# Performance work log

Measured on AMD Instinct MI355X. Metric: run time of the kernel, lower is better.

## Reference

```python
import jax, jax.numpy as jnp
import numpy as np

# ---- DNC configuration (mirrors access_config / controller_config / args) ----
T, B, IN, OUT = 64, 32, 64, 64          # time, batch, input_size, output_size
N, Wd, R, NW = 128, 64, 4, 1            # memory_size, word_size, num_reads, num_writes
H = 256                                  # controller hidden_size (2 LSTM layers)
CLIP = 20.0
EPS = 1e-6
NUM_MODES = 2 * NW + 1                   # backward modes, forward modes, content mode
IF_SIZES = [R*Wd, R, NW*Wd, NW, NW*Wd, NW*Wd, R, NW, NW, R*NUM_MODES]
IF_SIZE = int(np.sum(IF_SIZES))


def setup_inputs() -> dict:
    key = jax.random.key(0)
    ks = jax.random.split(key, 12)
    in0 = IN + R * Wd  # controller input = external input + flattened prev reads

    def w(k, shape, fan):
        return jax.random.normal(k, shape, jnp.float32) / np.float32(np.sqrt(fan))

    return {
        "inputs": jax.random.normal(ks[0], (T, B, IN), jnp.float32),
        "Wx0": w(ks[1], (in0, 4 * H), in0),
        "Wh0": w(ks[2], (H, 4 * H), H),
        "b0": jnp.zeros((4 * H,), jnp.float32),
        "Wx1": w(ks[3], (H, 4 * H), H),
        "Wh1": w(ks[4], (H, 4 * H), H),
        "b1": jnp.zeros((4 * H,), jnp.float32),
        "W_if": w(ks[5], (H, IF_SIZE), H),
        "b_if": jnp.zeros((IF_SIZE,), jnp.float32),
        "W_out": w(ks[6], (H + R * Wd, OUT), H + R * Wd),
        "b_out": jnp.zeros((OUT,), jnp.float32),
    }


def _lstm(x, h, c, Wx, Wh, b):
    g = x @ Wx + h @ Wh + b
    i, f, gg, o = jnp.split(g, 4, axis=-1)
    c2 = jax.nn.sigmoid(f) * c + jax.nn.sigmoid(i) * jnp.tanh(gg)
    h2 = jax.nn.sigmoid(o) * jnp.tanh(c2)
    return h2, c2


def _content_weights(memory, keys, strengths):
    # memory [B,N,W], keys [B,h,W], strengths [B,h] -> [B,h,N]
    mnorm = jnp.linalg.norm(memory, axis=-1)          # [B,N]
    knorm = jnp.linalg.norm(keys, axis=-1)            # [B,h]
    dot = jnp.einsum('bhw,bnw->bhn', keys, memory)
    sim = dot / (knorm[..., None] * mnorm[:, None, :] + EPS)
    return jax.nn.softmax(sim * strengths[..., None], axis=-1)


def _allocation(usage):
    # usage [B,N] -> allocation weighting [B,N] (DNC freeness-based)
    usage = EPS + (1.0 - EPS) * usage
    order = jnp.argsort(usage, axis=-1)               # ascending usage (most free first)
    sorted_usage = jnp.take_along_axis(usage, order, axis=-1)
    prod = jnp.cumprod(sorted_usage, axis=-1)
    prod_excl = jnp.concatenate([jnp.ones_like(prod[:, :1]), prod[:, :-1]], axis=-1)
    alloc_sorted = (1.0 - sorted_usage) * prod_excl
    inv = jnp.argsort(order, axis=-1)
    return jnp.take_along_axis(alloc_sorted, inv, axis=-1)


def _dnc_forward(inputs, Wx0, Wh0, b0, Wx1, Wh1, b1, W_if, b_if, W_out, b_out):
    eye = 1.0 - jnp.eye(N, dtype=jnp.float32)
    splits = np.cumsum(IF_SIZES)[:-1]

    def step(state, x_t):
        h0, c0, h1, c1, M, rw, ww, link, prec, usage, reads = state
        ctrl_in = jnp.concatenate([x_t, reads.reshape(B, R * Wd)], axis=-1)
        h0, c0 = _lstm(ctrl_in, h0, c0, Wx0, Wh0, b0)
        h1, c1 = _lstm(h0, h1, c1, Wx1, Wh1, b1)
        ctrl = jnp.clip(h1, -CLIP, CLIP)

        p = jnp.split(ctrl @ W_if + b_if, splits, axis=-1)
        read_keys = p[0].reshape(B, R, Wd)
        read_str = 1.0 + jax.nn.softplus(p[1])              # oneplus
        write_keys = p[2].reshape(B, NW, Wd)
        write_str = 1.0 + jax.nn.softplus(p[3])
        erase = jax.nn.sigmoid(p[4]).reshape(B, NW, Wd)
        write_vec = p[5].reshape(B, NW, Wd)
        free_g = jax.nn.sigmoid(p[6])                       # [B,R]
        alloc_g = jax.nn.sigmoid(p[7])                      # [B,NW]
        write_g = jax.nn.sigmoid(p[8])                      # [B,NW]
        modes = jax.nn.softmax(p[9].reshape(B, R, NUM_MODES), axis=-1)

        # -- usage update (prev write weights, then free gates on prev reads) --
        cw = 1.0 - jnp.prod(1.0 - ww, axis=1)               # [B,N]
        u = usage + (1.0 - usage) * cw
        psi = jnp.prod(1.0 - free_g[..., None] * rw, axis=1)
        usage = u * psi

        # -- write weights: content + allocation, gated --
        wc = _content_weights(M, write_keys, write_str)     # [B,NW,N]
        u_tmp = usage
        ww_heads = []
        for i in range(NW):
            a = _allocation(u_tmp)
            wg = write_g[:, i:i+1]
            ag = alloc_g[:, i:i+1]
            ww_heads.append(wg * (ag * a + (1.0 - ag) * wc[:, i]))
            u_tmp = u_tmp + (1.0 - u_tmp) * wg * a
        ww = jnp.stack(ww_heads, axis=1)                    # [B,NW,N]

        # -- erase + write memory --
        erase_m = jnp.prod(1.0 - ww[..., None] * erase[:, :, None, :], axis=1)  # [B,N,W]
        add_m = jnp.einsum('bwn,bwk->bnk', ww, write_vec)
        M = M * erase_m + add_m

        # -- temporal link matrix + precedence --
        wi = ww[..., :, None]
        wj = ww[..., None, :]
        link = ((1.0 - wi - wj) * link + wi * prec[..., None, :]) * eye
        prec = (1.0 - ww.sum(axis=-1, keepdims=True)) * prec + ww

        # -- read weights: backward / content / forward modes --
        rc = _content_weights(M, read_keys, read_str)       # [B,R,N]
        fwd = jnp.einsum('bwij,brj->brwi', link, rw)
        bwd = jnp.einsum('bwji,brj->brwi', link, rw)
        bmode = modes[..., :NW]
        fmode = modes[..., NW:2*NW]
        cmode = modes[..., 2*NW]
        rw = (jnp.einsum('brw,brwn->brn', bmode, bwd)
              + cmode[..., None] * rc
              + jnp.einsum('brw,brwn->brn', fmode, fwd))
        reads = jnp.einsum('brn,bnk->brk', rw, M)           # [B,R,W]

        out = jnp.clip(jnp.concatenate([ctrl, reads.reshape(B, R * Wd)], axis=-1) @ W_out + b_out,
                       -CLIP, CLIP)
        return (h0, c0, h1, c1, M, rw, ww, link, prec, usage, reads), out

    z = jnp.zeros
    init = (z((B, H)), z((B, H)), z((B, H)), z((B, H)),
            z((B, N, Wd)), z((B, R, N)), z((B, NW, N)),
            z((B, NW, N, N)), z((B, NW, N)), z((B, N)), z((B, R, Wd)))
    _, outs = jax.lax.scan(step, init, inputs)
    return outs                                            # [T,B,OUT]


def reference(inputs, Wx0, Wh0, b0, Wx1, Wh1, b1, W_if, b_if, W_out, b_out):
    return _dnc_forward(inputs, Wx0, Wh0, b0, Wx1, Wh1, b1, W_if, b_if, W_out, b_out)
```

## Files before the change

kernel.cpp:

```cpp
#include <hip/hip_runtime.h>
#include <math.h>


#define TT   64
#define BB   32
#define INW  64
#define OUTW 64
#define NN   128
#define WD   64
#define RR   4
#define HH   256
#define IFSZ 471
#define CLIPV 20.0f
#define EPSV  1e-6f
#define NBLK 96

#define OFF_RK   0
#define OFF_RSTR 256
#define OFF_WK   260
#define OFF_WSTR 324
#define OFF_ER   325
#define OFF_WV   389
#define OFF_FG   453
#define OFF_AG   457
#define OFF_WG   458
#define OFF_MD   459

#define S_WSTR 0
#define S_AG   1
#define S_WG   2
#define S_KNW  3
#define S_WSUM 4
#define S_RSTR 8
#define S_FG   12
#define S_KNR  16
#define S_BM   20
#define S_FM   24
#define S_CM   28

#define A_XS   0
#define A_GL   11840
#define A_C0   12896
#define A_GO   13152
#define A_WS   13216
#define A_WO   34528
#define B_XS   0
#define B_GL   9472
#define B_C1   10528
#define B_W1   10784
#define C_MS   0
#define C_LS   8320
#define C_WW   24832
#define C_PRC  24960
#define C_USG  25088
#define C_RWS  25216
#define C_IFC  25728
#define C_FWD  26208
#define C_BWD  26720
#define C_U2   27232
#define C_WCS  27360
#define C_RCS  27488
#define C_MNO  28000
#define C_RDS  28128
#define C_ERS  28384
#define C_WVS  28448
#define C_SC   28512
#define C_SCAL 28576

#define SMEM_FLOATS 36064
#define SMEM_BYTES  (SMEM_FLOATS*4)

#define W_CTL  0
#define W_RDS  8192
#define W_H0   16384
#define W_H1   32768
#define W_FLA  49152
#define W_FLB  (W_FLA + 1024)
#define W_FLC  (W_FLB + 1024)
#define W_END  (W_FLC + 1024)

__device__ __forceinline__ float sigf(float x){ return 1.0f/(1.0f+expf(-x)); }
__device__ __forceinline__ float sofp(float x){ return fmaxf(x,0.0f)+log1pf(expf(-fabsf(x))); }

__device__ __forceinline__ float gload(const float* p){
  return __hip_atomic_load(p, __ATOMIC_RELAXED, __HIP_MEMORY_SCOPE_AGENT);
}
__device__ __forceinline__ void gstore(float* p, float v){
  __hip_atomic_store(p, v, __ATOMIC_RELAXED, __HIP_MEMORY_SCOPE_AGENT);
}

__device__ __forceinline__ void waitflag(const unsigned* slots, unsigned target){
  if (threadIdx.x < 64){
    for (;;){
      unsigned m = __hip_atomic_load(&slots[(threadIdx.x & 31)*32],
                                     __ATOMIC_RELAXED, __HIP_MEMORY_SCOPE_AGENT);
      #pragma unroll
      for (int s=32;s>0;s>>=1){
        unsigned o = (unsigned)__shfl_xor((int)m, s, 64);
        m = (o < m) ? o : m;
      }
      if (m >= target) break;
      __builtin_amdgcn_s_sleep(2);
    }
  }
  __syncthreads();
}

__device__ __forceinline__ void setflag(unsigned* slots, int g, unsigned val){
  asm volatile("s_waitcnt vmcnt(0)" ::: "memory");
  __syncthreads();
  if (threadIdx.x == 0)
    __hip_atomic_store(&slots[g*32], val, __ATOMIC_RELAXED, __HIP_MEMORY_SCOPE_AGENT);
}

__device__ __forceinline__ float wredSum(float v){
  #pragma unroll
  for (int m=32;m>0;m>>=1) v += __shfl_xor(v,m,64);
  return v;
}
__device__ __forceinline__ float wredMax(float v){
  #pragma unroll
  for (int m=32;m>0;m>>=1) v = fmaxf(v,__shfl_xor(v,m,64));
  return v;
}

__device__ __forceinline__ float bfly64(float (&A)[64], int l, int* jb){
  #pragma unroll
  for (int st=0; st<6; ++st){
    const int m = 1<<st, half = 32>>st;
    const bool hi = (l & m) != 0;
    #pragma unroll
    for (int j=0;j<half;j++){
      float a = A[j], b = A[j+half];
      float keep = hi? b : a;
      float send = hi? a : b;
      A[j] = keep + __shfl_xor(send, m, 64);
    }
  }
  *jb = ((l&1)?32:0)|((l&2)?16:0)|((l&4)?8:0)|((l&8)?4:0)|((l&16)?2:0)|((l&32)?1:0);
  return A[0];
}

#define TILE_FMA(WBASE, WROW, XROW)                                      \
  {                                                                      \
    float xv[8], wv[8];                                                  \
    _Pragma("unroll")                                                    \
    for (int q=0;q<8;q++){                                               \
      wv[q] = sm[(WBASE) + (WROW)*37 + c0 + q];                          \
      xv[q] = Xs[(XROW)*37 + b0 + q];                                    \
    }                                                                    \
    _Pragma("unroll")                                                    \
    for (int bi=0;bi<8;bi++)                                             \
      _Pragma("unroll")                                                  \
      for (int ci=0;ci<8;ci++)                                           \
        acc[bi*8+ci] += xv[bi]*wv[ci];                                   \
  }

extern "C" __global__ __launch_bounds__(1024, 1)
void dnc_coop8(const float* __restrict__ inputs,
               const float* __restrict__ Wx0, const float* __restrict__ Wh0, const float* __restrict__ b0g,
               const float* __restrict__ Wx1, const float* __restrict__ Wh1, const float* __restrict__ b1g,
               const float* __restrict__ Wifg, const float* __restrict__ bifg,
               const float* __restrict__ Woutg, const float* __restrict__ boutg,
               float* __restrict__ outg, float* __restrict__ ws)
{
  const int bid  = blockIdx.x;
  const int role = bid >> 5;
  const int g    = bid & 31;
  const int tid  = threadIdx.x;
  const int lane = tid & 63;
  const int wid  = tid >> 6;

  extern __shared__ float sm[];

  float* gctl  = ws + W_CTL;
  float* greads= ws + W_RDS;
  unsigned* fA = (unsigned*)(ws + W_FLA);
  unsigned* fB = (unsigned*)(ws + W_FLB);
  unsigned* fC = (unsigned*)(ws + W_FLC);

  if (role == 0){
    for (int i = tid; i < 576*32; i += 1024){
      int r = i >> 5, cl = i & 31;
      int cglob = 8*g + (cl&7) + ((cl>>3)<<8);
      float v;
      if (r < 256)      v = Wx0[(64+r)*1024 + cglob];
      else if (r < 320) v = Wx0[(r-256)*1024 + cglob];
      else              v = Wh0[(r-320)*1024 + cglob];
      sm[A_WS + r*37 + cl] = v;
    }
    for (int i = tid; i < 512*2; i += 1024){
      int k = i >> 1, c = i & 1;
      sm[A_WO + k*3 + c] = Woutg[k*64 + 2*g + c];
    }
    if (tid < 256) sm[A_C0 + tid] = 0.0f;
  } else if (role == 1){
    for (int i = tid; i < 512*32; i += 1024){
      int r = i >> 5, cl = i & 31;
      int cglob = 8*g + (cl&7) + ((cl>>3)<<8);
      sm[B_W1 + r*37 + cl] = (r < 256) ? Wx1[r*1024 + cglob]
                                       : Wh1[(r-256)*1024 + cglob];
    }
    if (tid < 256) sm[B_C1 + tid] = 0.0f;
  } else {
    for (int i = tid; i < NN*65;  i += 1024) sm[C_MS + i] = 0.0f;
    for (int i = tid; i < NN*129; i += 1024) sm[C_LS + i] = 0.0f;
    if (tid < 128){ sm[C_WW+tid]=0.f; sm[C_PRC+tid]=0.f; sm[C_USG+tid]=0.f; }
    if (tid < 512) sm[C_RWS+tid]=0.f;
  }
  __syncthreads();

  if (role == 0){
    float* Xs = sm + A_XS;
    for (int t = 0; t <= TT; ++t){
      float* h0old = ws + W_H0 + (t&1)*8192;
      float* h0new = ws + W_H0 + ((t+1)&1)*8192;
      float acc[64]; float accO[16];

      waitflag(fA, (unsigned)t);
      if (t < TT){
        for (int i = tid; i < 256*32; i += 1024){
          int k = i>>5, bb = i&31; Xs[k*37+bb] = gload(&h0old[i]);
        }
        for (int i = tid; i < 64*32; i += 1024){
          int bb = i>>6, k = i&63;
          Xs[(256+k)*37+bb] = inputs[(t*BB + bb)*INW + k];
        }
        __syncthreads();
        #pragma unroll
        for (int j=0;j<64;j++) acc[j]=0.f;
        {
          const int b0 = (wid>>2)*8, c0 = (wid&3)*8;
          #pragma unroll
          for (int i=0;i<4;i++){
            int k = i*64 + lane;
            TILE_FMA(A_WS, 320+k, k)
          }
          TILE_FMA(A_WS, 256+lane, 256+lane)
        }
        __syncthreads();
      }
      if (t > 0){
        waitflag(fB, (unsigned)t);
        for (int i = tid; i < 256*32; i += 1024){
          int k = i>>5, bb = i&31; Xs[k*37+bb] = gload(&gctl[i]);
        }
        __syncthreads();
        #pragma unroll
        for (int j=0;j<16;j++) accO[j]=0.f;
        if (wid < 4){
          const int b0 = wid*8;
          #pragma unroll
          for (int i=0;i<4;i++){
            int k = i*64 + lane;
            float w0 = sm[A_WO + k*3], w1 = sm[A_WO + k*3 + 1];
            float xv[8];
            #pragma unroll
            for (int q=0;q<8;q++) xv[q] = Xs[k*37 + b0 + q];
            #pragma unroll
            for (int bi=0;bi<8;bi++){
              accO[bi*2]   += xv[bi]*w0;
              accO[bi*2+1] += xv[bi]*w1;
            }
          }
        }
        __syncthreads();
      }
      waitflag(fC, (unsigned)t);
      for (int i = tid; i < 256*32; i += 1024){
        int k = i>>5, bb = i&31; Xs[k*37+bb] = gload(&greads[i]);
      }
      __syncthreads();
      if (t > 0){
        if (wid < 4){
          const int b0 = wid*8;
          #pragma unroll
          for (int i=0;i<4;i++){
            int k = i*64 + lane;
            float w0 = sm[A_WO + (256+k)*3], w1 = sm[A_WO + (256+k)*3 + 1];
            float xv[8];
            #pragma unroll
            for (int q=0;q<8;q++) xv[q] = Xs[k*37 + b0 + q];
            #pragma unroll
            for (int bi=0;bi<8;bi++){
              accO[bi*2]   += xv[bi]*w0;
              accO[bi*2+1] += xv[bi]*w1;
            }
          }
          #pragma unroll
          for (int st=0; st<4; ++st){
            const int m = 1<<st, half = 8>>st;
            const bool hi = (lane & m) != 0;
            #pragma unroll
            for (int j=0;j<half;j++){
              float a = accO[j], b = accO[j+half];
              float keep = hi? b : a;
              float send = hi? a : b;
              accO[j] = keep + __shfl_xor(send, m, 64);
            }
          }
          accO[0] += __shfl_xor(accO[0], 16, 64);
          accO[0] += __shfl_xor(accO[0], 32, 64);
          int jb = ((lane&1)?8:0)|((lane&2)?4:0)|((lane&4)?2:0)|((lane&8)?1:0);
          if ((lane & 48) == 0){
            int bi = jb>>1, ci = jb&1;
            sm[A_GO + (wid*8+bi)*2 + ci] = accO[0];
          }
        }
        __syncthreads();
        if (tid < 64){
          int bb = tid>>1, c = tid&1;
          float v = sm[A_GO + tid] + boutg[2*g + c];
          outg[((t-1)*BB + bb)*OUTW + 2*g + c] = fminf(CLIPV, fmaxf(-CLIPV, v));
        }
      }
      if (t == TT) break;
      {
        const int b0 = (wid>>2)*8, c0 = (wid&3)*8;
        #pragma unroll
        for (int i=0;i<4;i++){
          int k = i*64 + lane;
          TILE_FMA(A_WS, k, k)
        }
        int jb; float v = bfly64(acc, lane, &jb);
        sm[A_GL + (b0 + (jb>>3))*33 + c0 + (jb&7)] = v;
      }
      __syncthreads();
      if (tid < 256){
        int bb = tid>>3, j = tid&7;
        float gi = sm[A_GL + bb*33 + j]      + b0g[8*g + j];
        float gf = sm[A_GL + bb*33 + 8 + j]  + b0g[256 + 8*g + j];
        float gg = sm[A_GL + bb*33 + 16 + j] + b0g[512 + 8*g + j];
        float go = sm[A_GL + bb*33 + 24 + j] + b0g[768 + 8*g + j];
        float c = sigf(gf)*sm[A_C0+tid] + sigf(gi)*tanhf(gg);
        sm[A_C0+tid] = c;
        gstore(&h0new[(8*g + j)*32 + bb], sigf(go)*tanhf(c));
      }
      setflag(fA, g, (unsigned)(t+1));
    }
  } else if (role == 1){
    float* Xs = sm + B_XS;
    for (int t = 0; t < TT; ++t){
      float* h0new = ws + W_H0 + ((t+1)&1)*8192;
      float* h1old = ws + W_H1 + (t&1)*8192;
      float* h1new = ws + W_H1 + ((t+1)&1)*8192;
      float acc[64];
      #pragma unroll
      for (int j=0;j<64;j++) acc[j]=0.f;

      waitflag(fB, (unsigned)t);
      for (int i = tid; i < 256*32; i += 1024){
        int k = i>>5, bb = i&31; Xs[k*37+bb] = gload(&h1old[i]);
      }
      __syncthreads();
      {
        const int b0 = (wid>>2)*8, c0 = (wid&3)*8;
        #pragma unroll
        for (int i=0;i<4;i++){
          int k = i*64 + lane;
          TILE_FMA(B_W1, 256+k, k)
        }
      }
      __syncthreads();
      waitflag(fA, (unsigned)(t+1));
      for (int i = tid; i < 256*32; i += 1024){
        int k = i>>5, bb = i&31; Xs[k*37+bb] = gload(&h0new[i]);
      }
      __syncthreads();
      {
        const int b0 = (wid>>2)*8, c0 = (wid&3)*8;
        #pragma unroll
        for (int i=0;i<4;i++){
          int k = i*64 + lane;
          TILE_FMA(B_W1, k, k)
        }
        int jb; float v = bfly64(acc, lane, &jb);
        sm[B_GL + (b0 + (jb>>3))*33 + c0 + (jb&7)] = v;
      }
      __syncthreads();
      if (tid < 256){
        int bb = tid>>3, j = tid&7;
        float gi = sm[B_GL + bb*33 + j]      + b1g[8*g + j];
        float gf = sm[B_GL + bb*33 + 8 + j]  + b1g[256 + 8*g + j];
        float gg = sm[B_GL + bb*33 + 16 + j] + b1g[512 + 8*g + j];
        float go = sm[B_GL + bb*33 + 24 + j] + b1g[768 + 8*g + j];
        float c = sigf(gf)*sm[B_C1+tid] + sigf(gi)*tanhf(gg);
        sm[B_C1+tid] = c;
        float h = sigf(go)*tanhf(c);
        gstore(&h1new[(8*g + j)*32 + bb], h);
        gstore(&gctl[(8*g + j)*32 + bb], fminf(CLIPV, fmaxf(-CLIPV, h)));
      }
      setflag(fB, g, (unsigned)(t+1));
    }
  } else {
    float* Ms  = sm + C_MS;
    float* Ls  = sm + C_LS;
    float* wws = sm + C_WW;
    float* prc = sm + C_PRC;
    float* usg = sm + C_USG;
    float* rws = sm + C_RWS;
    float* ifcl= sm + C_IFC;
    float* fwds= sm + C_FWD;
    float* bwds= sm + C_BWD;
    float* u2  = sm + C_U2;
    float* wcs = sm + C_WCS;
    float* rcs = sm + C_RCS;
    float* mno = sm + C_MNO;
    float* rds = sm + C_RDS;
    float* ers = sm + C_ERS;
    float* wvs = sm + C_WVS;
    float* sc  = sm + C_SC;
    float* scal= sm + C_SCAL;
    float* ctl_l = sm + C_RCS;
    float* part  = sm + C_FWD;

    for (int t = 0; t < TT; ++t){
      if (tid < 128){
        int n=tid; float s=0.f;
        #pragma unroll 8
        for (int d=0;d<WD;d++){ float v=Ms[n*65+d]; s+=v*v; }
        mno[n]=sqrtf(s);
      }
      waitflag(fB, (unsigned)(t+1));
      if (tid < 256) ctl_l[tid] = gload(&gctl[tid*32 + g]);
      __syncthreads();
      {
        const int kq = tid >> 9, c = tid & 511;
        if (c < IFSZ){
          const float* Wp = Wifg + (size_t)(kq*128)*IFSZ + c;
          const float* xp = ctl_l + kq*128;
          float a0=0.f, a1=0.f;
          #pragma unroll 8
          for (int k=0;k<128;k+=2){
            a0 += xp[k]   * Wp[(size_t)k*IFSZ];
            a1 += xp[k+1] * Wp[(size_t)(k+1)*IFSZ];
          }
          part[kq*512 + c] = a0 + a1;
        }
      }
      __syncthreads();
      if (tid < IFSZ) ifcl[tid] = part[tid] + part[512+tid] + bifg[tid];
      __syncthreads();

      if (tid < RR){
        scal[S_RSTR+tid]=1.0f+sofp(ifcl[OFF_RSTR+tid]);
        scal[S_FG+tid]  =sigf(ifcl[OFF_FG+tid]);
        float m0=ifcl[OFF_MD+tid*3], m1=ifcl[OFF_MD+tid*3+1], m2=ifcl[OFF_MD+tid*3+2];
        float mx=fmaxf(m0,fmaxf(m1,m2));
        float e0=expf(m0-mx), e1=expf(m1-mx), e2=expf(m2-mx);
        float s=e0+e1+e2;
        scal[S_BM+tid]=e0/s; scal[S_FM+tid]=e1/s; scal[S_CM+tid]=e2/s;
      }
      if (tid == 4) scal[S_WSTR]=1.0f+sofp(ifcl[OFF_WSTR]);
      if (tid == 5) scal[S_AG]=sigf(ifcl[OFF_AG]);
      if (tid == 6) scal[S_WG]=sigf(ifcl[OFF_WG]);
      if (tid >= 64 && tid < 128){
        int d=tid-64;
        ers[d]=sigf(ifcl[OFF_ER+d]);
        wvs[d]=ifcl[OFF_WV+d];
      }
      if (wid == 8){
        float v=ifcl[OFF_WK+lane]; float s=wredSum(v*v);
        if (lane==0) scal[S_KNW]=sqrtf(s);
      }
      if (wid >= 10 && wid < 14){
        int r=wid-10; float v=ifcl[OFF_RK+r*WD+lane]; float s=wredSum(v*v);
        if (lane==0) scal[S_KNR+r]=sqrtf(s);
      }
      __syncthreads();
      if (tid < NN){
        float dot=0.f;
        #pragma unroll 8
        for (int d=0;d<WD;d++) dot += ifcl[OFF_WK+d]*Ms[tid*65+d];
        float sim = dot/(scal[S_KNW]*mno[tid]+EPSV);
        wcs[tid]=sim*scal[S_WSTR];
      }
      __syncthreads();
      if (tid < NN){ float mx=wredMax(wcs[tid]); if(lane==0) sc[wid]=mx; }
      __syncthreads();
      if (tid < NN){
        float mx=fmaxf(sc[0],sc[1]);
        float e=expf(wcs[tid]-mx);
        wcs[tid]=e;
        float s=wredSum(e); if(lane==0) sc[2+wid]=s;
      }
      __syncthreads();
      if (tid < NN) wcs[tid]=wcs[tid]/(sc[2]+sc[3]);
      __syncthreads();
      if (tid < NN){
        float cw = wws[tid];
        float u  = usg[tid] + (1.0f-usg[tid])*cw;
        float psi=1.0f;
        #pragma unroll
        for (int r=0;r<RR;r++) psi *= 1.0f - scal[S_FG+r]*rws[r*NN+tid];
        float us = u*psi;
        usg[tid]=us;
        u2[tid] = EPSV + (1.0f-EPSV)*us;
      }
      __syncthreads();
      if (tid < NN){
        float ui=u2[tid]; float p=1.0f;
        for (int j=0;j<NN;j++){
          float uj=u2[j];
          bool take = (uj<ui) || (uj==ui && j<tid);
          p *= take ? uj : 1.0f;
        }
        float a = (1.0f-ui)*p;
        float wwn = scal[S_WG]*( scal[S_AG]*a + (1.0f-scal[S_AG])*wcs[tid] );
        wws[tid]=wwn;
        float s=wredSum(wwn); if(lane==0) sc[wid]=s;
      }
      __syncthreads();
      if (tid==0) scal[S_WSUM]=sc[0]+sc[1];
      __syncthreads();
      #pragma unroll
      for (int i=0;i<8;i++){
        int el=tid+i*1024, n=el>>6, d=el&63;
        float w=wws[n];
        Ms[n*65+d] = Ms[n*65+d]*(1.0f - w*ers[d]) + w*wvs[d];
      }
      #pragma unroll
      for (int i=0;i<16;i++){
        int el=tid+i*1024, li=el>>7, lj=el&127;
        float v = (li==lj) ? 0.0f
                : (1.0f - wws[li] - wws[lj])*Ls[li*129+lj] + wws[li]*prc[lj];
        Ls[li*129+lj]=v;
      }
      __syncthreads();
      if (tid < NN) prc[tid] = (1.0f - scal[S_WSUM])*prc[tid] + wws[tid];
      if (tid >= 128 && tid < 256){
        int n=tid-128; float s=0.f;
        #pragma unroll 8
        for (int d=0;d<WD;d++){ float v=Ms[n*65+d]; s+=v*v; }
        mno[n]=sqrtf(s);
      }
      __syncthreads();
      if (tid < RR*NN){
        int r=tid>>7, n=tid&127;
        float dot=0.f;
        #pragma unroll 8
        for (int d=0;d<WD;d++) dot += ifcl[OFF_RK+r*WD+d]*Ms[n*65+d];
        float sim = dot/(scal[S_KNR+r]*mno[n]+EPSV);
        rcs[tid]=sim*scal[S_RSTR+r];
      }
      __syncthreads();
      if (tid < RR*NN){ float mx=wredMax(rcs[tid]); if(lane==0) sc[wid]=mx; }
      __syncthreads();
      if (tid < RR*NN){
        int r=tid>>7;
        float mx=fmaxf(sc[r*2],sc[r*2+1]);
        float e=expf(rcs[tid]-mx);
        rcs[tid]=e;
        float s=wredSum(e); if(lane==0) sc[8+wid]=s;
      }
      __syncthreads();
      if (tid < RR*NN){
        int r=tid>>7;
        rcs[tid]=rcs[tid]/(sc[8+r*2]+sc[9+r*2]);
      }
      __syncthreads();
      if (tid < RR*NN){
        int r=tid>>7, i=tid&127;
        float f=0.f, bw=0.f;
        const float* rwr = rws + r*NN;
        #pragma unroll 4
        for (int j=0;j<NN;j++){
          float rv=rwr[j];
          f  += Ls[i*129+j]*rv;
          bw += Ls[j*129+i]*rv;
        }
        fwds[tid]=f; bwds[tid]=bw;
      }
      __syncthreads();
      if (tid < RR*NN){
        int r=tid>>7;
        rws[tid] = scal[S_BM+r]*bwds[tid] + scal[S_CM+r]*rcs[tid] + scal[S_FM+r]*fwds[tid];
      }
      __syncthreads();
      if (tid < RR*WD){
        int r=tid>>6, d=tid&63;
        float s=0.f;
        #pragma unroll 8
        for (int n=0;n<NN;n++) s += rws[r*NN+n]*Ms[n*65+d];
        rds[tid]=s;
      }
      __syncthreads();
      if (tid < 256) gstore(&greads[tid*32 + g], rds[tid]);
      setflag(fC, g, (unsigned)(t+1));
    }
  }
}

extern "C" void kernel_launch(void* const* d_in, const int* in_sizes, int n_in,
                              void* d_out, int out_size, void* d_ws, size_t ws_size,
                              hipStream_t stream)
{
  const float* inputs=(const float*)d_in[0];
  const float* Wx0   =(const float*)d_in[1];
  const float* Wh0   =(const float*)d_in[2];
  const float* b0    =(const float*)d_in[3];
  const float* Wx1   =(const float*)d_in[4];
  const float* Wh1   =(const float*)d_in[5];
  const float* b1    =(const float*)d_in[6];
  const float* Wif   =(const float*)d_in[7];
  const float* bif   =(const float*)d_in[8];
  const float* Wout  =(const float*)d_in[9];
  const float* bout  =(const float*)d_in[10];
  float* out = (float*)d_out;
  float* ws  = (float*)d_ws;

  hipMemsetAsync(ws, 0, W_END * sizeof(float), stream);

  hipFuncSetAttribute((const void*)dnc_coop8,
                      hipFuncAttributeMaxDynamicSharedMemorySize, SMEM_BYTES);

  void* args[] = { (void*)&inputs, (void*)&Wx0, (void*)&Wh0, (void*)&b0,
                   (void*)&Wx1, (void*)&Wh1, (void*)&b1, (void*)&Wif,
                   (void*)&bif, (void*)&Wout, (void*)&bout, (void*)&out,
                   (void*)&ws };
  hipLaunchCooperativeKernel((void*)dnc_coop8, dim3(NBLK), dim3(1024),
                             args, SMEM_BYTES, stream);
}
```

Measured before the change: 3.352 ms.

## Cut barriers in DNC memory step and reorder layer-0 LSTM before output

The memory role's per-step serial chain is restructured. Write and read content softmaxes now run per wavefront using shuffle reductions, independent scalar, usage and erase work runs concurrently in separate waves, memory and link updates are split across wave halves, and forward/backward link products overlap the read content weights. This removes many __syncthreads from the critical recurrent path. In the controller role, layer-0 LSTM for the next step is computed and flagged before the output projection, so downstream blocks can start earlier.

Result: slower. 3.642 ms (+8.7%).

```diff
diff --git a/kernel.cpp b/kernel.cpp
--- a/kernel.cpp
+++ b/kernel.cpp
@@ -26,14 +26,9 @@
 #define OFF_WG   458
 #define OFF_MD   459
 
-#define S_WSTR 0
 #define S_AG   1
 #define S_WG   2
-#define S_KNW  3
 #define S_WSUM 4
-#define S_RSTR 8
-#define S_FG   12
-#define S_KNR  16
 #define S_BM   20
 #define S_FM   24
 #define S_CM   28
@@ -61,10 +56,8 @@
 #define C_WCS  27360
 #define C_RCS  27488
 #define C_MNO  28000
-#define C_RDS  28128
 #define C_ERS  28384
 #define C_WVS  28448
-#define C_SC   28512
 #define C_SCAL 28576
 
 #define SMEM_FLOATS 36064
@@ -113,14 +106,14 @@
     __hip_atomic_store(&slots[g*32], val, __ATOMIC_RELAXED, __HIP_MEMORY_SCOPE_AGENT);
 }
 
-__device__ __forceinline__ float wredSum(float v){
+__device__ __forceinline__ float wmax64(float v){
+  #pragma unroll
+  for (int m=32;m>0;m>>=1) v = fmaxf(v, __shfl_xor(v,m,64));
+  return v;
+}
+__device__ __forceinline__ float wsum64(float v){
   #pragma unroll
   for (int m=32;m>0;m>>=1) v += __shfl_xor(v,m,64);
-  return v;
-}
-__device__ __forceinline__ float wredMax(float v){
-  #pragma unroll
-  for (int m=32;m>0;m>>=1) v = fmaxf(v,__shfl_xor(v,m,64));
   return v;
 }
 
@@ -157,7 +150,7 @@
   }
 
 extern "C" __global__ __launch_bounds__(1024, 1)
-void dnc_coop8(const float* __restrict__ inputs,
+void dnc_coop9(const float* __restrict__ inputs,
                const float* __restrict__ Wx0, const float* __restrict__ Wh0, const float* __restrict__ b0g,
                const float* __restrict__ Wx1, const float* __restrict__ Wh1, const float* __restrict__ b1g,
                const float* __restrict__ Wifg, const float* __restrict__ bifg,
@@ -271,6 +264,30 @@
         int k = i>>5, bb = i&31; Xs[k*37+bb] = gload(&greads[i]);
       }
       __syncthreads();
+      if (t < TT){
+        {
+          const int b0 = (wid>>2)*8, c0 = (wid&3)*8;
+          #pragma unroll
+          for (int i=0;i<4;i++){
+            int k = i*64 + lane;
+            TILE_FMA(A_WS, k, k)
+          }
+          int jb; float v = bfly64(acc, lane, &jb);
+          sm[A_GL + (b0 + (jb>>3))*33 + c0 + (jb&7)] = v;
+        }
+        __syncthreads();
+        if (tid < 256){
+          int bb = tid>>3, j = tid&7;
+          float gi = sm[A_GL + bb*33 + j]      + b0g[8*g + j];
+          float gf = sm[A_GL + bb*33 + 8 + j]  + b0g[256 + 8*g + j];
+          float gg = sm[A_GL + bb*33 + 16 + j] + b0g[512 + 8*g + j];
+          float go = sm[A_GL + bb*33 + 24 + j] + b0g[768 + 8*g + j];
+          float c = sigf(gf)*sm[A_C0+tid] + sigf(gi)*tanhf(gg);
+          sm[A_C0+tid] = c;
+          gstore(&h0new[(8*g + j)*32 + bb], sigf(go)*tanhf(c));
+        }
+        setflag(fA, g, (unsigned)(t+1));
+      }
       if (t > 0){
         if (wid < 4){
           const int b0 = wid*8;
@@ -314,29 +331,6 @@
           outg[((t-1)*BB + bb)*OUTW + 2*g + c] = fminf(CLIPV, fmaxf(-CLIPV, v));
         }
       }
-      if (t == TT) break;
-      {
-        const int b0 = (wid>>2)*8, c0 = (wid&3)*8;
-        #pragma unroll
-        for (int i=0;i<4;i++){
-          int k = i*64 + lane;
-          TILE_FMA(A_WS, k, k)
-        }
-        int jb; float v = bfly64(acc, lane, &jb);
-        sm[A_GL + (b0 + (jb>>3))*33 + c0 + (jb&7)] = v;
-      }
-      __syncthreads();
-      if (tid < 256){
-        int bb = tid>>3, j = tid&7;
-        float gi = sm[A_GL + bb*33 + j]      + b0g[8*g + j];
-        float gf = sm[A_GL + bb*33 + 8 + j]  + b0g[256 + 8*g + j];
-        float gg = sm[A_GL + bb*33 + 16 + j] + b0g[512 + 8*g + j];
-        float go = sm[A_GL + bb*33 + 24 + j] + b0g[768 + 8*g + j];
-        float c = sigf(gf)*sm[A_C0+tid] + sigf(gi)*tanhf(gg);
-        sm[A_C0+tid] = c;
-        gstore(&h0new[(8*g + j)*32 + bb], sigf(go)*tanhf(c));
-      }
-      setflag(fA, g, (unsigned)(t+1));
     }
   } else if (role == 1){
     float* Xs = sm + B_XS;
@@ -406,20 +400,18 @@
     float* wcs = sm + C_WCS;
     float* rcs = sm + C_RCS;
     float* mno = sm + C_MNO;
-    float* rds = sm + C_RDS;
     float* ers = sm + C_ERS;
     float* wvs = sm + C_WVS;
-    float* sc  = sm + C_SC;
     float* scal= sm + C_SCAL;
     float* ctl_l = sm + C_RCS;
     float* part  = sm + C_FWD;
 
     for (int t = 0; t < TT; ++t){
       if (tid < 128){
-        int n=tid; float s=0.f;
+        float s=0.f;
         #pragma unroll 8
-        for (int d=0;d<WD;d++){ float v=Ms[n*65+d]; s+=v*v; }
-        mno[n]=sqrtf(s);
+        for (int d=0;d<WD;d++){ float v=Ms[tid*65+d]; s+=v*v; }
+        mno[tid]=sqrtf(s);
       }
       waitflag(fB, (unsigned)(t+1));
       if (tid < 256) ctl_l[tid] = gload(&gctl[tid*32 + g]);
@@ -442,150 +434,138 @@
       if (tid < IFSZ) ifcl[tid] = part[tid] + part[512+tid] + bifg[tid];
       __syncthreads();
 
-      if (tid < RR){
-        scal[S_RSTR+tid]=1.0f+sofp(ifcl[OFF_RSTR+tid]);
-        scal[S_FG+tid]  =sigf(ifcl[OFF_FG+tid]);
-        float m0=ifcl[OFF_MD+tid*3], m1=ifcl[OFF_MD+tid*3+1], m2=ifcl[OFF_MD+tid*3+2];
-        float mx=fmaxf(m0,fmaxf(m1,m2));
-        float e0=expf(m0-mx), e1=expf(m1-mx), e2=expf(m2-mx);
-        float s=e0+e1+e2;
-        scal[S_BM+tid]=e0/s; scal[S_FM+tid]=e1/s; scal[S_CM+tid]=e2/s;
-      }
-      if (tid == 4) scal[S_WSTR]=1.0f+sofp(ifcl[OFF_WSTR]);
-      if (tid == 5) scal[S_AG]=sigf(ifcl[OFF_AG]);
-      if (tid == 6) scal[S_WG]=sigf(ifcl[OFF_WG]);
-      if (tid >= 64 && tid < 128){
-        int d=tid-64;
-        ers[d]=sigf(ifcl[OFF_ER+d]);
-        wvs[d]=ifcl[OFF_WV+d];
-      }
-      if (wid == 8){
-        float v=ifcl[OFF_WK+lane]; float s=wredSum(v*v);
-        if (lane==0) scal[S_KNW]=sqrtf(s);
-      }
-      if (wid >= 10 && wid < 14){
-        int r=wid-10; float v=ifcl[OFF_RK+r*WD+lane]; float s=wredSum(v*v);
-        if (lane==0) scal[S_KNR+r]=sqrtf(s);
-      }
-      __syncthreads();
-      if (tid < NN){
-        float dot=0.f;
+      if (wid == 0){
+        int n1 = lane, n2 = lane + 64;
+        float d1=0.f, d2=0.f, kn=0.f;
         #pragma unroll 8
-        for (int d=0;d<WD;d++) dot += ifcl[OFF_WK+d]*Ms[tid*65+d];
-        float sim = dot/(scal[S_KNW]*mno[tid]+EPSV);
-        wcs[tid]=sim*scal[S_WSTR];
-      }
-      __syncthreads();
-      if (tid < NN){ float mx=wredMax(wcs[tid]); if(lane==0) sc[wid]=mx; }
-      __syncthreads();
-      if (tid < NN){
-        float mx=fmaxf(sc[0],sc[1]);
-        float e=expf(wcs[tid]-mx);
-        wcs[tid]=e;
-        float s=wredSum(e); if(lane==0) sc[2+wid]=s;
-      }
-      __syncthreads();
-      if (tid < NN) wcs[tid]=wcs[tid]/(sc[2]+sc[3]);
-      __syncthreads();
-      if (tid < NN){
-        float cw = wws[tid];
-        float u  = usg[tid] + (1.0f-usg[tid])*cw;
-        float psi=1.0f;
+        for (int d=0; d<WD; ++d){
+          float wk = ifcl[OFF_WK+d];
+          d1 += wk*Ms[n1*65+d];
+          d2 += wk*Ms[n2*65+d];
+          kn += wk*wk;
+        }
+        float wstr = 1.0f + sofp(ifcl[OFF_WSTR]);
+        float knr = sqrtf(kn);
+        float s1 = d1/(knr*mno[n1]+EPSV)*wstr;
+        float s2 = d2/(knr*mno[n2]+EPSV)*wstr;
+        float mx = wmax64(fmaxf(s1,s2));
+        float e1 = expf(s1-mx), e2 = expf(s2-mx);
+        float sum = wsum64(e1+e2);
+        wcs[n1] = e1/sum; wcs[n2] = e2/sum;
+      } else if (wid == 1){
+        if (lane < 4){
+          float m0=ifcl[OFF_MD+lane*3], m1=ifcl[OFF_MD+lane*3+1], m2=ifcl[OFF_MD+lane*3+2];
+          float mx=fmaxf(m0,fmaxf(m1,m2));
+          float e0=expf(m0-mx), e1=expf(m1-mx), e2=expf(m2-mx);
+          float s=e0+e1+e2;
+          scal[S_BM+lane]=e0/s; scal[S_FM+lane]=e1/s; scal[S_CM+lane]=e2/s;
+        }
+        if (lane == 4) scal[S_AG]=sigf(ifcl[OFF_AG]);
+        if (lane == 5) scal[S_WG]=sigf(ifcl[OFF_WG]);
+      } else if (wid == 2 || wid == 3){
+        int n = tid - 128;
+        float cw = wws[n];
+        float u  = usg[n] + (1.0f-usg[n])*cw;
+        float psi = 1.0f;
         #pragma unroll
-        for (int r=0;r<RR;r++) psi *= 1.0f - scal[S_FG+r]*rws[r*NN+tid];
+        for (int r=0;r<RR;r++) psi *= 1.0f - sigf(ifcl[OFF_FG+r])*rws[r*NN+n];
         float us = u*psi;
-        usg[tid]=us;
-        u2[tid] = EPSV + (1.0f-EPSV)*us;
-      }
-      __syncthreads();
-      if (tid < NN){
-        float ui=u2[tid]; float p=1.0f;
+        usg[n] = us;
+        u2[n]  = EPSV + (1.0f-EPSV)*us;
+      } else if (wid == 4){
+        ers[lane] = sigf(ifcl[OFF_ER+lane]);
+        wvs[lane] = ifcl[OFF_WV+lane];
+      }
+      __syncthreads();
+
+      if (wid == 0){
+        int n1 = lane, n2 = lane + 64;
+        float uA = u2[n1], uB = u2[n2];
+        float p1 = 1.0f, p2 = 1.0f;
         for (int j=0;j<NN;j++){
-          float uj=u2[j];
-          bool take = (uj<ui) || (uj==ui && j<tid);
-          p *= take ? uj : 1.0f;
-        }
-        float a = (1.0f-ui)*p;
-        float wwn = scal[S_WG]*( scal[S_AG]*a + (1.0f-scal[S_AG])*wcs[tid] );
-        wws[tid]=wwn;
-        float s=wredSum(wwn); if(lane==0) sc[wid]=s;
-      }
-      __syncthreads();
-      if (tid==0) scal[S_WSUM]=sc[0]+sc[1];
-      __syncthreads();
-      #pragma unroll
-      for (int i=0;i<8;i++){
-        int el=tid+i*1024, n=el>>6, d=el&63;
-        float w=wws[n];
-        Ms[n*65+d] = Ms[n*65+d]*(1.0f - w*ers[d]) + w*wvs[d];
-      }
-      #pragma unroll
-      for (int i=0;i<16;i++){
-        int el=tid+i*1024, li=el>>7, lj=el&127;
-        float v = (li==lj) ? 0.0f
-                : (1.0f - wws[li] - wws[lj])*Ls[li*129+lj] + wws[li]*prc[lj];
-        Ls[li*129+lj]=v;
-      }
-      __syncthreads();
-      if (tid < NN) prc[tid] = (1.0f - scal[S_WSUM])*prc[tid] + wws[tid];
-      if (tid >= 128 && tid < 256){
-        int n=tid-128; float s=0.f;
+          float uj = u2[j];
+          p1 *= ((uj<uA)||(uj==uA && j<n1)) ? uj : 1.0f;
+          p2 *= ((uj<uB)||(uj==uB && j<n2)) ? uj : 1.0f;
+        }
+        float ag = scal[S_AG], wg = scal[S_WG];
+        float a1 = (1.0f-uA)*p1, a2 = (1.0f-uB)*p2;
+        float w1 = wg*(ag*a1 + (1.0f-ag)*wcs[n1]);
+        float w2 = wg*(ag*a2 + (1.0f-ag)*wcs[n2]);
+        wws[n1]=w1; wws[n2]=w2;
+        float s = wsum64(w1+w2);
+        if (lane==0) scal[S_WSUM]=s;
+      }
+      __syncthreads();
+
+      if (wid < 8){
+        #pragma unroll
+        for (int i=0;i<16;i++){
+          int el = tid + i*512, n = el>>6, d = el&63;
+          float w = wws[n];
+          Ms[n*65+d] = Ms[n*65+d]*(1.0f - w*ers[d]) + w*wvs[d];
+        }
+      } else {
+        int tt2 = tid - 512;
+        #pragma unroll
+        for (int i=0;i<32;i++){
+          int el = tt2 + i*512, li = el>>7, lj = el&127;
+          float v = (li==lj) ? 0.0f
+                  : (1.0f - wws[li] - wws[lj])*Ls[li*129+lj] + wws[li]*prc[lj];
+          Ls[li*129+lj] = v;
+        }
+      }
+      __syncthreads();
+
+      if (wid < 4){
+        const int r = wid;
+        int n1 = lane, n2 = lane + 64;
+        float d1=0.f, d2=0.f, kn=0.f, q1=0.f, q2=0.f;
         #pragma unroll 8
-        for (int d=0;d<WD;d++){ float v=Ms[n*65+d]; s+=v*v; }
-        mno[n]=sqrtf(s);
-      }
-      __syncthreads();
-      if (tid < RR*NN){
-        int r=tid>>7, n=tid&127;
-        float dot=0.f;
-        #pragma unroll 8
-        for (int d=0;d<WD;d++) dot += ifcl[OFF_RK+r*WD+d]*Ms[n*65+d];
-        float sim = dot/(scal[S_KNR+r]*mno[n]+EPSV);
-        rcs[tid]=sim*scal[S_RSTR+r];
-      }
-      __syncthreads();
-      if (tid < RR*NN){ float mx=wredMax(rcs[tid]); if(lane==0) sc[wid]=mx; }
-      __syncthreads();
-      if (tid < RR*NN){
-        int r=tid>>7;
-        float mx=fmaxf(sc[r*2],sc[r*2+1]);
-        float e=expf(rcs[tid]-mx);
-        rcs[tid]=e;
-        float s=wredSum(e); if(lane==0) sc[8+wid]=s;
-      }
-      __syncthreads();
-      if (tid < RR*NN){
-        int r=tid>>7;
-        rcs[tid]=rcs[tid]/(sc[8+r*2]+sc[9+r*2]);
-      }
-      __syncthreads();
-      if (tid < RR*NN){
-        int r=tid>>7, i=tid&127;
+        for (int d=0; d<WD; ++d){
+          float rk = ifcl[OFF_RK + r*WD + d];
+          float m1 = Ms[n1*65+d], m2 = Ms[n2*65+d];
+          d1 += rk*m1; d2 += rk*m2;
+          kn += rk*rk; q1 += m1*m1; q2 += m2*m2;
+        }
+        float rstr = 1.0f + sofp(ifcl[OFF_RSTR+r]);
+        float knr = sqrtf(kn);
+        float s1 = d1/(knr*sqrtf(q1)+EPSV)*rstr;
+        float s2 = d2/(knr*sqrtf(q2)+EPSV)*rstr;
+        float mx = wmax64(fmaxf(s1,s2));
+        float e1 = expf(s1-mx), e2 = expf(s2-mx);
+        float sum = wsum64(e1+e2);
+        rcs[r*NN+n1] = e1/sum; rcs[r*NN+n2] = e2/sum;
+      } else if (wid >= 8){
+        int idx = tid - 512, r = idx>>7, i = idx&127;
         float f=0.f, bw=0.f;
         const float* rwr = rws + r*NN;
         #pragma unroll 4
         for (int j=0;j<NN;j++){
-          float rv=rwr[j];
+          float rv = rwr[j];
           f  += Ls[i*129+j]*rv;
           bw += Ls[j*129+i]*rv;
         }
-        fwds[tid]=f; bwds[tid]=bw;
-      }
-      __syncthreads();
+        fwds[idx]=f; bwds[idx]=bw;
+      } else if (wid == 4){
+        float wsm = scal[S_WSUM];
+        prc[lane]    = (1.0f-wsm)*prc[lane]    + wws[lane];
+        prc[lane+64] = (1.0f-wsm)*prc[lane+64] + wws[lane+64];
+      }
+      __syncthreads();
+
       if (tid < RR*NN){
-        int r=tid>>7;
+        int r = tid>>7;
         rws[tid] = scal[S_BM+r]*bwds[tid] + scal[S_CM+r]*rcs[tid] + scal[S_FM+r]*fwds[tid];
       }
       __syncthreads();
+
       if (tid < RR*WD){
-        int r=tid>>6, d=tid&63;
+        int r = tid>>6, d = tid&63;
         float s=0.f;
         #pragma unroll 8
         for (int n=0;n<NN;n++) s += rws[r*NN+n]*Ms[n*65+d];
-        rds[tid]=s;
-      }
-      __syncthreads();
-      if (tid < 256) gstore(&greads[tid*32 + g], rds[tid]);
+        gstore(&greads[tid*32 + g], s);
+      }
       setflag(fC, g, (unsigned)(t+1));
     }
   }
@@ -611,13 +591,13 @@
 
   hipMemsetAsync(ws, 0, W_END * sizeof(float), stream);
 
-  hipFuncSetAttribute((const void*)dnc_coop8,
+  hipFuncSetAttribute((const void*)dnc_coop9,
                       hipFuncAttributeMaxDynamicSharedMemorySize, SMEM_BYTES);
 
   void* args[] = { (void*)&inputs, (void*)&Wx0, (void*)&Wh0, (void*)&b0,
                    (void*)&Wx1, (void*)&Wh1, (void*)&b1, (void*)&Wif,
                    (void*)&bif, (void*)&Wout, (void*)&bout, (void*)&out,
                    (void*)&ws };
-  hipLaunchCooperativeKernel((void*)dnc_coop8, dim3(NBLK), dim3(1024),
+  hipLaunchCooperativeKernel((void*)dnc_coop9, dim3(NBLK), dim3(1024),
                              args, SMEM_BYTES, stream);
 }
```

## Fold LSTM layer 1 into per-batch memory blocks, dropping one pipeline stage

Applied to the files above, without the earlier changes.

Removes the 32 blocks that computed the second LSTM layer and moves that work into each per-batch memory block. Each memory block now computes its own batch's layer-1 gates by streaming Wx1/Wh1 from global memory with float4 loads. The aim is to cut one cross-block flag handoff and global exchange per timestep on the serial critical path. In exchange, each memory block reads the full 2MB of layer-1 weights from L2 every step instead of keeping a slice in LDS. Layer-0 compute is also reordered to run before the output projection so the next step can start sooner.

Result: slower. 5.370 ms (+60.2%).

```diff
diff --git a/kernel.cpp b/kernel.cpp
--- a/kernel.cpp
+++ b/kernel.cpp
@@ -13,7 +13,7 @@
 #define IFSZ 471
 #define CLIPV 20.0f
 #define EPSV  1e-6f
-#define NBLK 96
+#define NBLK 64
 
 #define OFF_RK   0
 #define OFF_RSTR 256
@@ -44,10 +44,6 @@
 #define A_GO   13152
 #define A_WS   13216
 #define A_WO   34528
-#define B_XS   0
-#define B_GL   9472
-#define B_C1   10528
-#define B_W1   10784
 #define C_MS   0
 #define C_LS   8320
 #define C_WW   24832
@@ -61,11 +57,14 @@
 #define C_WCS  27360
 #define C_RCS  27488
 #define C_MNO  28000
-#define C_RDS  28128
 #define C_ERS  28384
 #define C_WVS  28448
 #define C_SC   28512
 #define C_SCAL 28576
+#define C_HV   28608
+#define C_C1   29120
+#define C_CTL  29376
+#define C_PART 29632
 
 #define SMEM_FLOATS 36064
 #define SMEM_BYTES  (SMEM_FLOATS*4)
@@ -73,10 +72,9 @@
 #define W_CTL  0
 #define W_RDS  8192
 #define W_H0   16384
-#define W_H1   32768
 #define W_FLA  49152
-#define W_FLB  (W_FLA + 1024)
-#define W_FLC  (W_FLB + 1024)
+#define W_FLT  (W_FLA + 1024)
+#define W_FLC  (W_FLT + 1024)
 #define W_END  (W_FLC + 1024)
 
 __device__ __forceinline__ float sigf(float x){ return 1.0f/(1.0f+expf(-x)); }
@@ -157,12 +155,12 @@
   }
 
 extern "C" __global__ __launch_bounds__(1024, 1)
-void dnc_coop8(const float* __restrict__ inputs,
-               const float* __restrict__ Wx0, const float* __restrict__ Wh0, const float* __restrict__ b0g,
-               const float* __restrict__ Wx1, const float* __restrict__ Wh1, const float* __restrict__ b1g,
-               const float* __restrict__ Wifg, const float* __restrict__ bifg,
-               const float* __restrict__ Woutg, const float* __restrict__ boutg,
-               float* __restrict__ outg, float* __restrict__ ws)
+void dnc_coop10(const float* __restrict__ inputs,
+                const float* __restrict__ Wx0, const float* __restrict__ Wh0, const float* __restrict__ b0g,
+                const float* __restrict__ Wx1, const float* __restrict__ Wh1, const float* __restrict__ b1g,
+                const float* __restrict__ Wifg, const float* __restrict__ bifg,
+                const float* __restrict__ Woutg, const float* __restrict__ boutg,
+                float* __restrict__ outg, float* __restrict__ ws)
 {
   const int bid  = blockIdx.x;
   const int role = bid >> 5;
@@ -176,7 +174,7 @@
   float* gctl  = ws + W_CTL;
   float* greads= ws + W_RDS;
   unsigned* fA = (unsigned*)(ws + W_FLA);
-  unsigned* fB = (unsigned*)(ws + W_FLB);
+  unsigned* fCt= (unsigned*)(ws + W_FLT);
   unsigned* fC = (unsigned*)(ws + W_FLC);
 
   if (role == 0){
@@ -194,19 +192,13 @@
       sm[A_WO + k*3 + c] = Woutg[k*64 + 2*g + c];
     }
     if (tid < 256) sm[A_C0 + tid] = 0.0f;
-  } else if (role == 1){
-    for (int i = tid; i < 512*32; i += 1024){
-      int r = i >> 5, cl = i & 31;
-      int cglob = 8*g + (cl&7) + ((cl>>3)<<8);
-      sm[B_W1 + r*37 + cl] = (r < 256) ? Wx1[r*1024 + cglob]
-                                       : Wh1[(r-256)*1024 + cglob];
-    }
-    if (tid < 256) sm[B_C1 + tid] = 0.0f;
   } else {
     for (int i = tid; i < NN*65;  i += 1024) sm[C_MS + i] = 0.0f;
     for (int i = tid; i < NN*129; i += 1024) sm[C_LS + i] = 0.0f;
     if (tid < 128){ sm[C_WW+tid]=0.f; sm[C_PRC+tid]=0.f; sm[C_USG+tid]=0.f; }
     if (tid < 512) sm[C_RWS+tid]=0.f;
+    if (tid < 512) sm[C_HV+tid]=0.f;
+    if (tid < 256) sm[C_C1+tid]=0.f;
   }
   __syncthreads();
 
@@ -241,7 +233,7 @@
         __syncthreads();
       }
       if (t > 0){
-        waitflag(fB, (unsigned)t);
+        waitflag(fCt, (unsigned)t);
         for (int i = tid; i < 256*32; i += 1024){
           int k = i>>5, bb = i&31; Xs[k*37+bb] = gload(&gctl[i]);
         }
@@ -271,6 +263,30 @@
         int k = i>>5, bb = i&31; Xs[k*37+bb] = gload(&greads[i]);
       }
       __syncthreads();
+      if (t < TT){
+        {
+          const int b0 = (wid>>2)*8, c0 = (wid&3)*8;
+          #pragma unroll
+          for (int i=0;i<4;i++){
+            int k = i*64 + lane;
+            TILE_FMA(A_WS, k, k)
+          }
+          int jb; float v = bfly64(acc, lane, &jb);
+          sm[A_GL + (b0 + (jb>>3))*33 + c0 + (jb&7)] = v;
+        }
+        __syncthreads();
+        if (tid < 256){
+          int bb = tid>>3, j = tid&7;
+          float gi = sm[A_GL + bb*33 + j]      + b0g[8*g + j];
+          float gf = sm[A_GL + bb*33 + 8 + j]  + b0g[256 + 8*g + j];
+          float gg = sm[A_GL + bb*33 + 16 + j] + b0g[512 + 8*g + j];
+          float go = sm[A_GL + bb*33 + 24 + j] + b0g[768 + 8*g + j];
+          float c = sigf(gf)*sm[A_C0+tid] + sigf(gi)*tanhf(gg);
+          sm[A_C0+tid] = c;
+          gstore(&h0new[(8*g + j)*32 + bb], sigf(go)*tanhf(c));
+        }
+        setflag(fA, g, (unsigned)(t+1));
+      }
       if (t > 0){
         if (wid < 4){
           const int b0 = wid*8;
@@ -314,83 +330,6 @@
           outg[((t-1)*BB + bb)*OUTW + 2*g + c] = fminf(CLIPV, fmaxf(-CLIPV, v));
         }
       }
-      if (t == TT) break;
-      {
-        const int b0 = (wid>>2)*8, c0 = (wid&3)*8;
-        #pragma unroll
-        for (int i=0;i<4;i++){
-          int k = i*64 + lane;
-          TILE_FMA(A_WS, k, k)
-        }
-        int jb; float v = bfly64(acc, lane, &jb);
-        sm[A_GL + (b0 + (jb>>3))*33 + c0 + (jb&7)] = v;
-      }
-      __syncthreads();
-      if (tid < 256){
-        int bb = tid>>3, j = tid&7;
-        float gi = sm[A_GL + bb*33 + j]      + b0g[8*g + j];
-        float gf = sm[A_GL + bb*33 + 8 + j]  + b0g[256 + 8*g + j];
-        float gg = sm[A_GL + bb*33 + 16 + j] + b0g[512 + 8*g + j];
-        float go = sm[A_GL + bb*33 + 24 + j] + b0g[768 + 8*g + j];
-        float c = sigf(gf)*sm[A_C0+tid] + sigf(gi)*tanhf(gg);
-        sm[A_C0+tid] = c;
-        gstore(&h0new[(8*g + j)*32 + bb], sigf(go)*tanhf(c));
-      }
-      setflag(fA, g, (unsigned)(t+1));
-    }
-  } else if (role == 1){
-    float* Xs = sm + B_XS;
-    for (int t = 0; t < TT; ++t){
-      float* h0new = ws + W_H0 + ((t+1)&1)*8192;
-      float* h1old = ws + W_H1 + (t&1)*8192;
-      float* h1new = ws + W_H1 + ((t+1)&1)*8192;
-      float acc[64];
-      #pragma unroll
-      for (int j=0;j<64;j++) acc[j]=0.f;
-
-      waitflag(fB, (unsigned)t);
-      for (int i = tid; i < 256*32; i += 1024){
-        int k = i>>5, bb = i&31; Xs[k*37+bb] = gload(&h1old[i]);
-      }
-      __syncthreads();
-      {
-        const int b0 = (wid>>2)*8, c0 = (wid&3)*8;
-        #pragma unroll
-        for (int i=0;i<4;i++){
-          int k = i*64 + lane;
-          TILE_FMA(B_W1, 256+k, k)
-        }
-      }
-      __syncthreads();
-      waitflag(fA, (unsigned)(t+1));
-      for (int i = tid; i < 256*32; i += 1024){
-        int k = i>>5, bb = i&31; Xs[k*37+bb] = gload(&h0new[i]);
-      }
-      __syncthreads();
-      {
-        const int b0 = (wid>>2)*8, c0 = (wid&3)*8;
-        #pragma unroll
-        for (int i=0;i<4;i++){
-          int k = i*64 + lane;
-          TILE_FMA(B_W1, k, k)
-        }
-        int jb; float v = bfly64(acc, lane, &jb);
-        sm[B_GL + (b0 + (jb>>3))*33 + c0 + (jb&7)] = v;
-      }
-      __syncthreads();
-      if (tid < 256){
-        int bb = tid>>3, j = tid&7;
-        float gi = sm[B_GL + bb*33 + j]      + b1g[8*g + j];
-        float gf = sm[B_GL + bb*33 + 8 + j]  + b1g[256 + 8*g + j];
-        float gg = sm[B_GL + bb*33 + 16 + j] + b1g[512 + 8*g + j];
-        float go = sm[B_GL + bb*33 + 24 + j] + b1g[768 + 8*g + j];
-        float c = sigf(gf)*sm[B_C1+tid] + sigf(gi)*tanhf(gg);
-        sm[B_C1+tid] = c;
-        float h = sigf(go)*tanhf(c);
-        gstore(&h1new[(8*g + j)*32 + bb], h);
-        gstore(&gctl[(8*g + j)*32 + bb], fminf(CLIPV, fmaxf(-CLIPV, h)));
-      }
-      setflag(fB, g, (unsigned)(t+1));
     }
   } else {
     float* Ms  = sm + C_MS;
@@ -406,29 +345,65 @@
     float* wcs = sm + C_WCS;
     float* rcs = sm + C_RCS;
     float* mno = sm + C_MNO;
-    float* rds = sm + C_RDS;
     float* ers = sm + C_ERS;
     float* wvs = sm + C_WVS;
     float* sc  = sm + C_SC;
     float* scal= sm + C_SCAL;
-    float* ctl_l = sm + C_RCS;
-    float* part  = sm + C_FWD;
+    float* hvec= sm + C_HV;
+    float* c1l = sm + C_C1;
+    float* ctl = sm + C_CTL;
+    float* part= sm + C_PART;
 
     for (int t = 0; t < TT; ++t){
+      float* h0new = ws + W_H0 + ((t+1)&1)*8192;
+
       if (tid < 128){
-        int n=tid; float s=0.f;
+        float s=0.f;
         #pragma unroll 8
-        for (int d=0;d<WD;d++){ float v=Ms[n*65+d]; s+=v*v; }
-        mno[n]=sqrtf(s);
-      }
-      waitflag(fB, (unsigned)(t+1));
-      if (tid < 256) ctl_l[tid] = gload(&gctl[tid*32 + g]);
-      __syncthreads();
+        for (int d=0;d<WD;d++){ float v=Ms[tid*65+d]; s+=v*v; }
+        mno[tid]=sqrtf(s);
+      }
+      waitflag(fA, (unsigned)(t+1));
+      if (tid < 256) hvec[tid] = gload(&h0new[tid*32 + g]);
+      __syncthreads();
+      {
+        const int kq = tid >> 8, j4 = tid & 255;
+        const float* Wb = (kq < 2) ? (Wx1 + (size_t)(kq*128)*1024 + 4*j4)
+                                   : (Wh1 + (size_t)((kq-2)*128)*1024 + 4*j4);
+        const float* xp = hvec + kq*128;
+        float a0=0.f,a1=0.f,a2=0.f,a3=0.f;
+        #pragma unroll 8
+        for (int k=0;k<128;k++){
+          float4 w = *reinterpret_cast<const float4*>(Wb + (size_t)k*1024);
+          float x = xp[k];
+          a0 += x*w.x; a1 += x*w.y; a2 += x*w.z; a3 += x*w.w;
+        }
+        *reinterpret_cast<float4*>(&part[kq*1024 + 4*j4]) = make_float4(a0,a1,a2,a3);
+      }
+      __syncthreads();
+      if (tid < 256){
+        const int j = tid;
+        float gi=b1g[j], gf=b1g[256+j], gg=b1g[512+j], go=b1g[768+j];
+        #pragma unroll
+        for (int q=0;q<4;q++){
+          const float* pp = part + q*1024;
+          gi += pp[j]; gf += pp[256+j]; gg += pp[512+j]; go += pp[768+j];
+        }
+        float c = sigf(gf)*c1l[j] + sigf(gi)*tanhf(gg);
+        c1l[j] = c;
+        float h = sigf(go)*tanhf(c);
+        hvec[256+j] = h;
+        float cl = fminf(CLIPV, fmaxf(-CLIPV, h));
+        ctl[j] = cl;
+        gstore(&gctl[j*32 + g], cl);
+      }
+      setflag(fCt, g, (unsigned)(t+1));
+
       {
         const int kq = tid >> 9, c = tid & 511;
         if (c < IFSZ){
           const float* Wp = Wifg + (size_t)(kq*128)*IFSZ + c;
-          const float* xp = ctl_l + kq*128;
+          const float* xp = ctl + kq*128;
           float a0=0.f, a1=0.f;
           #pragma unroll 8
           for (int k=0;k<128;k+=2){
@@ -582,10 +557,8 @@
         float s=0.f;
         #pragma unroll 8
         for (int n=0;n<NN;n++) s += rws[r*NN+n]*Ms[n*65+d];
-        rds[tid]=s;
-      }
-      __syncthreads();
-      if (tid < 256) gstore(&greads[tid*32 + g], rds[tid]);
+        gstore(&greads[tid*32 + g], s);
+      }
       setflag(fC, g, (unsigned)(t+1));
     }
   }
@@ -611,13 +584,13 @@
 
   hipMemsetAsync(ws, 0, W_END * sizeof(float), stream);
 
-  hipFuncSetAttribute((const void*)dnc_coop8,
+  hipFuncSetAttribute((const void*)dnc_coop10,
                       hipFuncAttributeMaxDynamicSharedMemorySize, SMEM_BYTES);
 
   void* args[] = { (void*)&inputs, (void*)&Wx0, (void*)&Wh0, (void*)&b0,
                    (void*)&Wx1, (void*)&Wh1, (void*)&b1, (void*)&Wif,
                    (void*)&bif, (void*)&Wout, (void*)&bout, (void*)&out,
                    (void*)&ws };
-  hipLaunchCooperativeKernel((void*)dnc_coop8, dim3(NBLK), dim3(1024),
+  hipLaunchCooperativeKernel((void*)dnc_coop10, dim3(NBLK), dim3(1024),
                              args, SMEM_BYTES, stream);
 }
```
